# Performance work log

Measured on AMD Instinct MI355X. Metric: run time of the kernel, lower is better.

Reference implementation:

```python
import jax, jax.numpy as jnp
import numpy as np
import math

B, L, C, D, H, NL, DF, Z = 32, 256, 55, 512, 8, 3, 512, 16
DK = D // H


def setup_inputs() -> dict:
    key = jax.random.key(0)
    ks = iter(jax.random.split(key, 40))
    def w(shape, s=0.05):
        return jax.random.normal(next(ks), shape, jnp.float32) * s
    return {
        "x": jax.random.normal(next(ks), (B, L, C), jnp.float32),
        "tok_w": w((D, C, 3)),
        "qkv_w": w((NL, 3, D, D)), "qkv_b": w((NL, 3, D)),
        "sig_w": w((NL, H, D)), "sig_b": w((NL, H)),
        "out_w": w((NL, D, D)), "out_b": w((NL, D)),
        "conv1_w": w((NL, DF, D)), "conv1_b": w((NL, DF)),
        "conv2_w": w((NL, D, DF)), "conv2_b": w((NL, D)),
        "ln1_g": jnp.ones((NL, D)), "ln1_b": jnp.zeros((NL, D)),
        "ln2_g": jnp.ones((NL, D)), "ln2_b": jnp.zeros((NL, D)),
        "lnf_g": jnp.ones((D,)), "lnf_b": jnp.zeros((D,)),
        "lat_w": w((Z, D)), "lat_b": w((Z,)),
        "dec1_w": w((D, Z)), "dec1_b": w((D,)),
        "dec2_w": w((C, D)), "dec2_b": w((C,)),
    }


def _layer_norm(x, g, b, eps=1e-5):
    m = jnp.mean(x, axis=-1, keepdims=True)
    v = jnp.mean(jnp.square(x - m), axis=-1, keepdims=True)
    return (x - m) * jax.lax.rsqrt(v + eps) * g + b


def _pos_embedding(seq_len, d_model):
    pos = jnp.arange(seq_len, dtype=jnp.float32)[:, None]
    div = jnp.exp(jnp.arange(0, d_model, 2, dtype=jnp.float32) * (-math.log(10000.0) / d_model))
    pe = jnp.zeros((seq_len, d_model), jnp.float32)
    pe = pe.at[:, 0::2].set(jnp.sin(pos * div))
    pe = pe.at[:, 1::2].set(jnp.cos(pos * div))
    return pe  # (L, D)


def _token_embedding(x, tok_w):
    # torch Conv1d(C, D, k=3, padding=1, padding_mode='circular', bias=False)
    xp = jnp.pad(x, ((0, 0), (1, 1), (0, 0)), mode="wrap")  # circular pad on L
    k = jnp.transpose(tok_w, (2, 1, 0))  # (W=3, I=C, O=D)
    return jax.lax.conv_general_dilated(xp, k, (1,), "VALID",
                                        dimension_numbers=("NWC", "WIO", "NWC"))


def _forward(x, tok_w, qkv_w, qkv_b, sig_w, sig_b, out_w, out_b,
             conv1_w, conv1_b, conv2_w, conv2_b, ln1_g, ln1_b, ln2_g, ln2_b,
             lnf_g, lnf_b, lat_w, lat_b, dec1_w, dec1_b, dec2_w, dec2_b):
    Bx, Lx, _ = x.shape
    # DataEmbedding (dropout=0)
    h = _token_embedding(x, tok_w) + _pos_embedding(Lx, D)[None]
    dist = jnp.abs(jnp.arange(Lx, dtype=jnp.float32)[:, None]
                   - jnp.arange(Lx, dtype=jnp.float32)[None, :])  # (L, L)
    scale = 1.0 / math.sqrt(DK)
    series_list, prior_list = [], []
    for i in range(NL):
        # AttentionLayer projections
        q = (h @ qkv_w[i, 0].T + qkv_b[i, 0]).reshape(Bx, Lx, H, DK)
        k = (h @ qkv_w[i, 1].T + qkv_b[i, 1]).reshape(Bx, Lx, H, DK)
        v = (h @ qkv_w[i, 2].T + qkv_b[i, 2]).reshape(Bx, Lx, H, DK)
        sigma = h @ sig_w[i].T + sig_b[i]                 # (B, L, H)
        # AnomalyAttention
        scores = jnp.einsum("blhe,bshe->bhls", q, k) * scale
        series = jax.nn.softmax(scores, axis=-1)          # (B, H, L, L)
        sig = jnp.transpose(sigma, (0, 2, 1))             # (B, H, L)
        sig = jax.nn.sigmoid(sig * 5.0) + 1e-5
        sig = jnp.power(3.0, sig) - 1.0
        sig = sig[..., None]                              # (B, H, L, 1)
        prior = (1.0 / (math.sqrt(2.0 * math.pi) * sig)
                 * jnp.exp(-jnp.square(dist) / (2.0 * jnp.square(sig))))
        V = jnp.einsum("bhls,bshd->blhd", series, v).reshape(Bx, Lx, D)
        new_h = V @ out_w[i].T + out_b[i]
        # EncoderLayer (post-norm, pointwise-conv FFN, gelu)
        h = h + new_h
        y = h = _layer_norm(h, ln1_g[i], ln1_b[i])
        y = jax.nn.gelu(jnp.einsum("bld,fd->blf", y, conv1_w[i]) + conv1_b[i], approximate=False)
        y = jnp.einsum("blf,df->bld", y, conv2_w[i]) + conv2_b[i]
        h = _layer_norm(h + y, ln2_g[i], ln2_b[i])
        series_list.append(series)
        prior_list.append(prior)
    h = _layer_norm(h, lnf_g, lnf_b)
    z = h @ lat_w.T + lat_b                               # (B, L, Z)
    recon = jax.nn.relu(z @ dec1_w.T + dec1_b) @ dec2_w.T + dec2_b  # MLPDecoder
    return recon, jnp.stack(series_list), jnp.stack(prior_list), z


def reference(x, tok_w, qkv_w, qkv_b, sig_w, sig_b, out_w, out_b,
              conv1_w, conv1_b, conv2_w, conv2_b, ln1_g, ln1_b, ln2_g, ln2_b,
              lnf_g, lnf_b, lat_w, lat_b, dec1_w, dec1_b, dec2_w, dec2_b):
    return _forward(x, tok_w, qkv_w, qkv_b, sig_w, sig_b, out_w, out_b,
                    conv1_w, conv1_b, conv2_w, conv2_b, ln1_g, ln1_b, ln2_g, ln2_b,
                    lnf_g, lnf_b, lat_w, lat_b, dec1_w, dec1_b, dec2_w, dec2_b)
```

## Files before the change

### kernel.cpp

```cpp
#include <hip/hip_runtime.h>
#include <math.h>

#define B_ 32
#define L_ 256
#define C_ 55
#define D_ 512
#define H_ 8
#define NL_ 3
#define DF_ 512
#define Z_ 16
#define DK_ 64

typedef unsigned short u16;
typedef __attribute__((ext_vector_type(8))) short s16x8;
typedef __attribute__((ext_vector_type(8))) _Float16 f16x8;
typedef __attribute__((ext_vector_type(4))) float f32x4;

__device__ __forceinline__ u16 f2h(float f) {
  _Float16 h = (_Float16)f;
  return __builtin_bit_cast(u16, h);
}
__device__ __forceinline__ void gload16(const void* g, void* l) {
  __builtin_amdgcn_global_load_lds(
      (const __attribute__((address_space(1))) unsigned*)g,
      (__attribute__((address_space(3))) unsigned*)l, 16, 0, 0);
}

template <int MF, int WM, int WN, int ACT, int OUT>
__device__ __forceinline__ void mgemm_body(
    char* As, char* Bs, const u16* __restrict__ A16,
    const u16* __restrict__ B16, const float* __restrict__ bias,
    float* __restrict__ Cf, u16* __restrict__ C16, int K, int lda, int ldb,
    int ldc, int nmax, int bxi, int byi) {
  constexpr int BM = WM * MF * 16, BN = WN * 64, T = WM * WN * 64;
  constexpr int ACH = BM * 8, BCH = BN * 8;
  const int t = threadIdx.x, lane = t & 63, w = t >> 6;
  const int wm = w / WN, wn = w % WN;
  const long m0 = (long)byi * BM, n0 = (long)bxi * BN;
  const char* Ab = (const char*)(A16 + m0 * lda);
  const char* Bb = (const char*)(B16 + n0 * ldb);
  const int fr = lane & 15, gq = lane >> 4;
  const long lda2 = (long)lda * 2, ldb2 = (long)ldb * 2;
  f32x4 acc[MF][4] = {};
  for (int k0 = 0; k0 < K; k0 += 64) {
    const long kb = (long)k0 * 2;
#pragma unroll
    for (int e = 0; e < ACH; e += T) {
      int id = e + t;
      int row = id >> 3, c = (id & 7) ^ (row & 7);
      gload16(Ab + (long)row * lda2 + kb + c * 16, As + id * 16);
    }
#pragma unroll
    for (int e = 0; e < BCH; e += T) {
      int id = e + t;
      int row = id >> 3, c = (id & 7) ^ (row & 7);
      gload16(Bb + (long)row * ldb2 + kb + c * 16, Bs + id * 16);
    }
    __syncthreads();
#pragma unroll
    for (int ks = 0; ks < 2; ++ks) {
      f16x8 a[MF], b[4];
#pragma unroll
      for (int m = 0; m < MF; ++m) {
        int row = wm * (MF * 16) + m * 16 + fr;
        a[m] = *(const f16x8*)(As + row * 128 +
                               ((gq * 16 + ks * 64) ^ ((row & 7) << 4)));
      }
#pragma unroll
      for (int n = 0; n < 4; ++n) {
        int row = wn * 64 + n * 16 + fr;
        b[n] = *(const f16x8*)(Bs + row * 128 +
                               ((gq * 16 + ks * 64) ^ ((row & 7) << 4)));
      }
#pragma unroll
      for (int m = 0; m < MF; ++m)
#pragma unroll
        for (int n = 0; n < 4; ++n)
          acc[m][n] =
              __builtin_amdgcn_mfma_f32_16x16x32_f16(a[m], b[n], acc[m][n], 0, 0, 0);
    }
    __syncthreads();
  }
#pragma unroll
  for (int m = 0; m < MF; ++m) {
    long mg = m0 + wm * (MF * 16) + m * 16 + gq * 4;
#pragma unroll
    for (int n = 0; n < 4; ++n) {
      int ng = (int)n0 + wn * 64 + n * 16 + fr;
      if (ng >= nmax) continue;
      float bv = bias ? bias[ng] : 0.f;
#pragma unroll
      for (int r = 0; r < 4; ++r) {
        float v = acc[m][n][r] + bv;
        if (ACT == 1) v = 0.5f * v * (1.f + erff(v * 0.70710678118654752f));
        long idx = (mg + r) * ldc + ng;
        if (OUT == 0) Cf[idx] = v;
        if (OUT == 1) C16[idx] = f2h(v);
      }
    }
  }
}

template <int MF, int WM, int WN, int ACT, int OUT>
__global__ __launch_bounds__(WM * WN * 64) void mgemm(
    const u16* __restrict__ A16, const u16* __restrict__ B16,
    const float* __restrict__ bias, float* __restrict__ Cf,
    u16* __restrict__ C16, int K, int lda, int ldb, int ldc, int nmax) {
  __shared__ __align__(16) char As[WM * MF * 16 * 128];
  __shared__ __align__(16) char Bs[WN * 64 * 128];
  mgemm_body<MF, WM, WN, ACT, OUT>(As, Bs, A16, B16, bias, Cf, C16, K, lda,
                                   ldb, ldc, nmax, blockIdx.x, blockIdx.y);
}

__global__ __launch_bounds__(256) void qkv_kernel(
    const u16* __restrict__ h16, const u16* __restrict__ w16,
    const float* __restrict__ bias, u16* __restrict__ qk16,
    u16* __restrict__ vt16, const float* __restrict__ h32,
    const float* __restrict__ sw, const float* __restrict__ sb,
    float* __restrict__ coef, float* __restrict__ c2f) {
  __shared__ __align__(16) char As[128 * 128];
  __shared__ __align__(16) char Bs[128 * 128];
  __shared__ float sm[4][8];
  int bx = blockIdx.x;
  if (bx < 8192) {
    int bl = bx;
    int l = bl & 255, b = bl >> 8;
    int t = threadIdx.x;
    const float* hrow = h32 + (long)bl * 512;
    float h0 = hrow[t], h1 = hrow[t + 256];
    float part[8];
#pragma unroll
    for (int hd = 0; hd < 8; ++hd) {
      const float* wrow = sw + hd * 512;
      part[hd] = h0 * wrow[t] + h1 * wrow[t + 256];
    }
#pragma unroll
    for (int off = 32; off > 0; off >>= 1)
#pragma unroll
      for (int hd = 0; hd < 8; ++hd) part[hd] += __shfl_xor(part[hd], off, 64);
    int wid = t >> 6;
    if ((t & 63) == 0) {
#pragma unroll
      for (int hd = 0; hd < 8; ++hd) sm[wid][hd] = part[hd];
    }
    __syncthreads();
    if (t < 8) {
      float sig = sm[0][t] + sm[1][t] + sm[2][t] + sm[3][t] + sb[t];
      sig = 1.f / (1.f + expf(-5.f * sig));
      sig += 1e-5f;
      sig = expf(sig * 1.0986122886681098f) - 1.f;
      long idx = ((long)(b * 8 + t) << 8) | l;
      coef[idx] = 0.3989422804014327f / sig;
      c2f[idx] = -0.5f / (sig * sig);
    }
  } else if (bx < 8704) {
    int b2 = bx - 8192;
    mgemm_body<4, 2, 2, 0, 1>(As, Bs, h16, w16, bias, nullptr, qk16, 512, 512,
                              512, 1024, 1024, b2 & 7, b2 >> 3);
  } else {
    int b3 = bx - 8704;
    mgemm_body<2, 2, 2, 0, 1>(As, Bs, w16 + 1024 * 512, h16, nullptr, nullptr,
                              vt16, 512, 512, 512, 8192, 8192, b3 & 63,
                              b3 >> 6);
  }
}

__global__ __launch_bounds__(256, 2) void fused_attn(
    const u16* __restrict__ qk16, const u16* __restrict__ vt16,
    const float* __restrict__ vbias, const float* __restrict__ coef,
    const float* __restrict__ c2f, float* __restrict__ ser,
    float* __restrict__ pri, u16* __restrict__ pv16) {
  __shared__ __align__(16) char smem[67584];
  char* Kreg = smem;
  char* V0 = smem + 32768;
  char* V1 = smem + 49152;
  float* rowred = (float*)(smem + 65536);
  const int t = threadIdx.x, lane = t & 63, w = t >> 6;
  const int fr = lane & 15, gq = lane >> 4;
  const int r0 = blockIdx.x * 64;
  const int bh = blockIdx.y, b = bh >> 3, h = bh & 7;
  const long qrow0 = (long)b * 256 + r0;
  const long krow0 = (long)b * 256;
  {
    const char* qs = (const char*)qk16 + qrow0 * 2048 + h * 128;
#pragma unroll
    for (int j = 0; j < 2; ++j) {
      int id = t + j * 256;
      int row = id >> 3, c = id & 7;
      *(s16x8*)(V0 + row * 144 + c * 16) =
          *(const s16x8*)(qs + (long)row * 2048 + c * 16);
    }
  }
  const char* kb = (const char*)qk16 + krow0 * 2048 + 1024 + h * 128;
#pragma unroll
  for (int j = 0; j < 8; ++j) {
    int id = t + j * 256;
    int row = id >> 3, c = (id & 7) ^ (row & 7);
    gload16(kb + (long)row * 2048 + c * 16, Kreg + id * 16);
  }
  __syncthreads();
  f32x4 acc[4][4] = {};
#pragma unroll
  for (int ks = 0; ks < 2; ++ks) {
    f16x8 aq[4], bk[4];
#pragma unroll
    for (int m = 0; m < 4; ++m)
      aq[m] = *(const f16x8*)(V0 + (m * 16 + fr) * 144 + gq * 16 + ks * 64);
#pragma unroll
    for (int n = 0; n < 4; ++n) {
      int row = w * 64 + n * 16 + fr;
      bk[n] = *(const f16x8*)(Kreg + row * 128 +
                              ((gq * 16 + ks * 64) ^ ((row & 7) << 4)));
    }
#pragma unroll
    for (int m = 0; m < 4; ++m)
#pragma unroll
      for (int n = 0; n < 4; ++n)
        acc[m][n] =
            __builtin_amdgcn_mfma_f32_16x16x32_f16(aq[m], bk[n], acc[m][n], 0, 0, 0);
  }
#pragma unroll
  for (int m = 0; m < 4; ++m)
#pragma unroll
    for (int n = 0; n < 4; ++n) acc[m][n] *= 0.125f;
  float lmax[4][4], lsum[4][4];
#pragma unroll
  for (int m = 0; m < 4; ++m)
#pragma unroll
    for (int r = 0; r < 4; ++r) {
      float v = fmaxf(fmaxf(acc[m][0][r], acc[m][1][r]),
                      fmaxf(acc[m][2][r], acc[m][3][r]));
#pragma unroll
      for (int off = 8; off > 0; off >>= 1) v = fmaxf(v, __shfl_xor(v, off, 64));
      lmax[m][r] = v;
    }
#pragma unroll
  for (int m = 0; m < 4; ++m)
#pragma unroll
    for (int n = 0; n < 4; ++n)
#pragma unroll
      for (int r = 0; r < 4; ++r)
        acc[m][n][r] = __expf(acc[m][n][r] - lmax[m][r]);
#pragma unroll
  for (int m = 0; m < 4; ++m)
#pragma unroll
    for (int r = 0; r < 4; ++r) {
      float s = acc[m][0][r] + acc[m][1][r] + acc[m][2][r] + acc[m][3][r];
#pragma unroll
      for (int off = 8; off > 0; off >>= 1) s += __shfl_xor(s, off, 64);
      lsum[m][r] = s;
    }
  if (fr == 0) {
#pragma unroll
    for (int m = 0; m < 4; ++m)
#pragma unroll
      for (int r = 0; r < 4; ++r) {
        int row = m * 16 + gq * 4 + r;
        rowred[(w * 64 + row) * 2] = lmax[m][r];
        rowred[(w * 64 + row) * 2 + 1] = lsum[m][r];
      }
  }
  __syncthreads();
  float scale[4][4];
#pragma unroll
  for (int m = 0; m < 4; ++m)
#pragma unroll
    for (int r = 0; r < 4; ++r) {
      int row = m * 16 + gq * 4 + r;
      float g = -1e30f, tot = 0.f;
      float2 pr[4];
#pragma unroll
      for (int ww = 0; ww < 4; ++ww) {
        pr[ww] = *(const float2*)&rowred[(ww * 64 + row) * 2];
        g = fmaxf(g, pr[ww].x);
      }
#pragma unroll
      for (int ww = 0; ww < 4; ++ww) tot += pr[ww].y * __expf(pr[ww].x - g);
      scale[m][r] = __expf(lmax[m][r] - g) / tot;
    }
  const char* vtb = (const char*)vt16 + ((long)h * 64 * 8192 + krow0) * 2;
#pragma unroll
  for (int j = 0; j < 4; ++j) {
    int id = t + j * 256;
    int row = id >> 5, c = (id & 31) ^ (row & 7);
    gload16(vtb + (long)row * 16384 + c * 16, V0 + id * 16);
    gload16(vtb + (long)(32 + row) * 16384 + c * 16, V1 + id * 16);
  }
  float* serb = ser + ((long)bh * 256 + r0) * 256 + w * 64;
  float* prib = pri + ((long)bh * 256 + r0) * 256 + w * 64;
  const float* cfb = coef + bh * 256 + r0;
  const float* ccb = c2f + bh * 256 + r0;
#pragma unroll
  for (int m = 0; m < 4; ++m)
#pragma unroll
    for (int r = 0; r < 4; ++r) {
      int row = m * 16 + gq * 4 + r;
      float cf = cfb[row], cc = ccb[row];
      float fl = (float)(r0 + row);
#pragma unroll
      for (int n = 0; n < 4; ++n) {
        int col = n * 16 + fr;
        float p = acc[m][n][r] * scale[m][r];
        serb[(long)row * 256 + col] = p;
        int pb = row * 512 + (((w * 64 + col) * 2) ^ ((row & 7) << 4));
        *(u16*)(Kreg + pb) = f2h(p);
        float dd = fl - (float)(w * 64 + col);
        prib[(long)row * 256 + col] = cf * __expf(cc * dd * dd);
      }
    }
  __syncthreads();
  f32x4 acc2[2][2] = {};
#pragma unroll
  for (int ks = 0; ks < 8; ++ks) {
    int arow = w * 16 + fr;
    f16x8 pa = *(const f16x8*)(
        Kreg + arow * 512 + ((gq * 16 + ks * 64) ^ ((arow & 7) << 4)));
#pragma unroll
    for (int n = 0; n < 2; ++n) {
      int vrow = n * 16 + fr;
      int vo = vrow * 512 + ((gq * 16 + ks * 64) ^ ((vrow & 7) << 4));
      f16x8 vb0 = *(const f16x8*)(V0 + vo);
      f16x8 vb1 = *(const f16x8*)(V1 + vo);
      acc2[0][n] = __builtin_amdgcn_mfma_f32_16x16x32_f16(pa, vb0, acc2[0][n], 0, 0, 0);
      acc2[1][n] = __builtin_amdgcn_mfma_f32_16x16x32_f16(pa, vb1, acc2[1][n], 0, 0, 0);
    }
  }
#pragma unroll
  for (int half = 0; half < 2; ++half)
#pragma unroll
    for (int n = 0; n < 2; ++n)
#pragma unroll
      for (int r = 0; r < 4; ++r) {
        int gcol = h * 64 + half * 32 + n * 16 + fr;
        long gm = qrow0 + w * 16 + gq * 4 + r;
        pv16[gm * 512 + gcol] = f2h(acc2[half][n][r] + vbias[gcol]);
      }
}

template <int ACT, bool O16>
__global__ __launch_bounds__(256) void gemm_kernel(
    const float* __restrict__ A, const float* __restrict__ Bm,
    const float* __restrict__ bias, float* __restrict__ C,
    u16* __restrict__ C16, int M, int N, int K, int lda, int ldb, int ldc) {
  __shared__ float Asm[16][65];
  __shared__ float Bsm[16][65];
  int t = threadIdx.x;
  int tx = t & 15, ty = t >> 4;
  int n0 = blockIdx.x * 64, m0 = blockIdx.y * 64;
  float acc[4][4] = {};
  for (int k0 = 0; k0 < K; k0 += 16) {
#pragma unroll
    for (int e = 0; e < 4; ++e) {
      int idx = t + e * 256;
      int mi = idx >> 4, ki = idx & 15;
      int m = m0 + mi, kk = k0 + ki;
      Asm[ki][mi] = (m < M && kk < K) ? A[(long)m * lda + kk] : 0.f;
      int n = n0 + mi;
      Bsm[ki][mi] = (n < N && kk < K) ? Bm[(long)n * ldb + kk] : 0.f;
    }
    __syncthreads();
#pragma unroll
    for (int kk = 0; kk < 16; ++kk) {
      float a[4], b[4];
#pragma unroll
      for (int i = 0; i < 4; ++i) a[i] = Asm[kk][ty + 16 * i];
#pragma unroll
      for (int j = 0; j < 4; ++j) b[j] = Bsm[kk][tx + 16 * j];
#pragma unroll
      for (int i = 0; i < 4; ++i)
#pragma unroll
        for (int j = 0; j < 4; ++j) acc[i][j] = fmaf(a[i], b[j], acc[i][j]);
    }
    __syncthreads();
  }
#pragma unroll
  for (int i = 0; i < 4; ++i) {
    int m = m0 + ty + 16 * i;
    if (m >= M) continue;
#pragma unroll
    for (int j = 0; j < 4; ++j) {
      int n = n0 + tx + 16 * j;
      if (n >= N) continue;
      float v = acc[i][j];
      if (bias) v += bias[n];
      if (ACT == 2) v = fmaxf(v, 0.f);
      if (O16)
        C16[(long)m * ldc + n] = f2h(v);
      else
        C[(long)m * ldc + n] = v;
    }
  }
}

__global__ __launch_bounds__(256) void conv_embed_kernel(
    const float* __restrict__ x, const float* __restrict__ tw,
    const float* __restrict__ qkv_w, const float* __restrict__ out_w,
    const float* __restrict__ c1w, const float* __restrict__ c2w,
    const float* __restrict__ latw, const float* __restrict__ d2w,
    float* __restrict__ h32, u16* __restrict__ h16, u16* __restrict__ wqkv16,
    u16* __restrict__ wo16, u16* __restrict__ c116, u16* __restrict__ c216,
    u16* __restrict__ latpad, u16* __restrict__ d2pad) {
  __shared__ float xs[18][56];
  int bx = blockIdx.x;
  int t = threadIdx.x;
  if (bx < 512) {
    int lt = (bx & 15) * 16;
    int b = bx >> 4;
    for (int idx = t; idx < 18 * 55; idx += 256) {
      int rr = idx / 55, cc = idx % 55;
      int gl = (lt + rr - 1 + L_) & (L_ - 1);
      xs[rr][cc] = x[(long)(b * L_ + gl) * C_ + cc];
    }
    __syncthreads();
    for (int dp = 0; dp < 2; ++dp) {
      int d = t + dp * 256;
      float acc[16] = {};
      const float* wr = tw + (long)d * (C_ * 3);
      for (int c = 0; c < C_; ++c) {
#pragma unroll
        for (int w = 0; w < 3; ++w) {
          float wv = wr[c * 3 + w];
#pragma unroll
          for (int l = 0; l < 16; ++l) acc[l] = fmaf(xs[l + w][c], wv, acc[l]);
        }
      }
      float ang_scale = expf(-(float)(d & ~1) * 0.017988946039015984f);
#pragma unroll
      for (int l = 0; l < 16; ++l) {
        float ang = (float)(lt + l) * ang_scale;
        float pe = (d & 1) ? cosf(ang) : sinf(ang);
        float v = acc[l] + pe;
        long idx = (long)(b * L_ + lt + l) * D_ + d;
        h32[idx] = v;
        h16[idx] = f2h(v);
      }
    }
    return;
  }
  int cb = bx - 512;
  if (cb < 9216) {
    int i = cb * 256 + t;
    wqkv16[i] = f2h(qkv_w[i]);
  } else if (cb < 12288) {
    int i = (cb - 9216) * 256 + t;
    wo16[i] = f2h(out_w[i]);
  } else if (cb < 15360) {
    int i = (cb - 12288) * 256 + t;
    c116[i] = f2h(c1w[i]);
  } else if (cb < 18432) {
    int i = (cb - 15360) * 256 + t;
    c216[i] = f2h(c2w[i]);
  } else if (cb < 18560) {
    int i = (cb - 18432) * 256 + t;
    int r = i >> 9, c = i & 511;
    latpad[i] = (r < Z_) ? f2h(latw[r * 512 + c]) : (u16)0;
  } else {
    int i = (cb - 18560) * 256 + t;
    int r = i >> 9, c = i & 511;
    d2pad[i] = (r < C_) ? f2h(d2w[r * 512 + c]) : (u16)0;
  }
}

__global__ __launch_bounds__(256) void lnw_kernel(
    const float* __restrict__ a, const float* __restrict__ r,
    const float* __restrict__ gg, const float* __restrict__ be,
    float* __restrict__ ofp, u16* __restrict__ o16,
    const float* __restrict__ g2, const float* __restrict__ b2) {
  int wave = threadIdx.x >> 6, lane = threadIdx.x & 63;
  long row = (long)blockIdx.x * 4 + wave;
  long base = row * D_ + lane * 8;
  int cb = lane * 8;
  f32x4 xa = *(const f32x4*)(a + base);
  f32x4 xb = *(const f32x4*)(a + base + 4);
  if (r) {
    xa += *(const f32x4*)(r + base);
    xb += *(const f32x4*)(r + base + 4);
  }
  float x[8] = {xa.x, xa.y, xa.z, xa.w, xb.x, xb.y, xb.z, xb.w};
  float s = 0.f;
#pragma unroll
  for (int e = 0; e < 8; ++e) s += x[e];
#pragma unroll
  for (int off = 32; off > 0; off >>= 1) s += __shfl_xor(s, off, 64);
  float mean = s * (1.f / D_);
  float vv = 0.f;
#pragma unroll
  for (int e = 0; e < 8; ++e) {
    x[e] -= mean;
    vv += x[e] * x[e];
  }
#pragma unroll
  for (int off = 32; off > 0; off >>= 1) vv += __shfl_xor(vv, off, 64);
  float rstd = rsqrtf(vv * (1.f / D_) + 1e-5f);
  f32x4 ga = *(const f32x4*)(gg + cb), gb = *(const f32x4*)(gg + cb + 4);
  f32x4 ba = *(const f32x4*)(be + cb), bb = *(const f32x4*)(be + cb + 4);
  float g[8] = {ga.x, ga.y, ga.z, ga.w, gb.x, gb.y, gb.z, gb.w};
  float bi[8] = {ba.x, ba.y, ba.z, ba.w, bb.x, bb.y, bb.z, bb.w};
  float v[8];
#pragma unroll
  for (int e = 0; e < 8; ++e) v[e] = x[e] * rstd * g[e] + bi[e];
  if (ofp) {
    f32x4 oa = {v[0], v[1], v[2], v[3]}, ob = {v[4], v[5], v[6], v[7]};
    *(f32x4*)(ofp + base) = oa;
    *(f32x4*)(ofp + base + 4) = ob;
  }
  if (g2) {
    float s2 = 0.f;
#pragma unroll
    for (int e = 0; e < 8; ++e) s2 += v[e];
#pragma unroll
    for (int off = 32; off > 0; off >>= 1) s2 += __shfl_xor(s2, off, 64);
    float mean2 = s2 * (1.f / D_);
    float vv2 = 0.f;
#pragma unroll
    for (int e = 0; e < 8; ++e) {
      v[e] -= mean2;
      vv2 += v[e] * v[e];
    }
#pragma unroll
    for (int off = 32; off > 0; off >>= 1) vv2 += __shfl_xor(vv2, off, 64);
    float rstd2 = rsqrtf(vv2 * (1.f / D_) + 1e-5f);
    f32x4 g2a = *(const f32x4*)(g2 + cb), g2b = *(const f32x4*)(g2 + cb + 4);
    f32x4 b2a = *(const f32x4*)(b2 + cb), b2b = *(const f32x4*)(b2 + cb + 4);
    float gg2[8] = {g2a.x, g2a.y, g2a.z, g2a.w, g2b.x, g2b.y, g2b.z, g2b.w};
    float bb2[8] = {b2a.x, b2a.y, b2a.z, b2a.w, b2b.x, b2b.y, b2b.z, b2b.w};
#pragma unroll
    for (int e = 0; e < 8; ++e) v[e] = v[e] * rstd2 * gg2[e] + bb2[e];
  }
  if (o16) {
    u16 h[8];
#pragma unroll
    for (int e = 0; e < 8; ++e) h[e] = f2h(v[e]);
    *(s16x8*)(o16 + base) = *(s16x8*)h;
  }
}

extern "C" void kernel_launch(void* const* d_in, const int* in_sizes, int n_in,
                              void* d_out, int out_size, void* d_ws,
                              size_t ws_size, hipStream_t stream) {
  (void)in_sizes; (void)n_in; (void)out_size; (void)ws_size;
  const float* x = (const float*)d_in[0];
  const float* tok_w = (const float*)d_in[1];
  const float* qkv_w = (const float*)d_in[2];
  const float* qkv_b = (const float*)d_in[3];
  const float* sig_w = (const float*)d_in[4];
  const float* sig_b = (const float*)d_in[5];
  const float* out_w = (const float*)d_in[6];
  const float* out_b = (const float*)d_in[7];
  const float* c1w = (const float*)d_in[8];
  const float* c1b = (const float*)d_in[9];
  const float* c2w = (const float*)d_in[10];
  const float* c2b = (const float*)d_in[11];
  const float* ln1g = (const float*)d_in[12];
  const float* ln1b = (const float*)d_in[13];
  const float* ln2g = (const float*)d_in[14];
  const float* ln2b = (const float*)d_in[15];
  const float* lnfg = (const float*)d_in[16];
  const float* lnfb = (const float*)d_in[17];
  const float* latw = (const float*)d_in[18];
  const float* latb = (const float*)d_in[19];
  const float* d1w = (const float*)d_in[20];
  const float* d1b = (const float*)d_in[21];
  const float* d2w = (const float*)d_in[22];
  const float* d2b = (const float*)d_in[23];
  float* out = (float*)d_out;

  const long BLD = (long)B_ * L_ * D_;
  const long CHUNK = (long)B_ * H_ * L_ * L_;
  const long SER_OFF = (long)B_ * L_ * C_;
  const long PRI_OFF = SER_OFF + NL_ * CHUNK;
  const long Z_OFF = PRI_OFF + NL_ * CHUNK;
  const int M = B_ * L_;
  const int DD = D_ * D_;

  char* wp = (char*)d_ws;
  auto alloc = [&](size_t bytes) {
    char* p = wp;
    wp += (bytes + 255) & ~(size_t)255;
    return p;
  };
  float* h32 = (float*)alloc(BLD * 4);
  u16* h16 = (u16*)alloc(BLD * 2);
  float* tb = (float*)alloc(BLD * 4);
  u16* qk16 = (u16*)alloc(BLD * 4);
  u16* vt16 = (u16*)alloc(BLD * 2);
  u16* pv16 = (u16*)alloc(BLD * 2);
  float* coef = (float*)alloc((size_t)B_ * H_ * L_ * 4);
  float* c2f = (float*)alloc((size_t)B_ * H_ * L_ * 4);
  u16* wqkv16 = (u16*)alloc((size_t)NL_ * 3 * DD * 2);
  u16* wo16 = (u16*)alloc((size_t)NL_ * DD * 2);
  u16* c116 = (u16*)alloc((size_t)NL_ * DD * 2);
  u16* c216 = (u16*)alloc((size_t)NL_ * DD * 2);
  u16* latpad = (u16*)alloc((size_t)64 * 512 * 2);
  u16* d2pad = (u16*)alloc((size_t)64 * 512 * 2);

  conv_embed_kernel<<<18688, 256, 0, stream>>>(
      x, tok_w, qkv_w, out_w, c1w, c2w, latw, d2w, h32, h16, wqkv16, wo16,
      c116, c216, latpad, d2pad);

  for (int i = 0; i < NL_; ++i) {
    const long ofQK = (long)(i * 3) * DD;
    qkv_kernel<<<9216, 256, 0, stream>>>(
        h16, wqkv16 + ofQK, qkv_b + (long)i * 3 * D_, qk16, vt16, h32,
        sig_w + (long)i * H_ * D_, sig_b + i * H_, coef, c2f);
    fused_attn<<<dim3(4, 256), 256, 0, stream>>>(
        qk16, vt16, qkv_b + (long)(i * 3 + 2) * D_, coef, c2f,
        out + SER_OFF + i * CHUNK, out + PRI_OFF + i * CHUNK, pv16);
    mgemm<2, 2, 1, 0, 0><<<dim3(8, 128), 128, 0, stream>>>(
        pv16, wo16 + (long)i * DD, out_b + i * D_, tb, nullptr, D_, D_, D_, D_,
        D_);
    lnw_kernel<<<M / 4, 256, 0, stream>>>(h32, tb, ln1g + i * D_,
                                          ln1b + i * D_, h32, h16, nullptr,
                                          nullptr);
    u16* y16 = qk16;
    mgemm<2, 2, 1, 1, 1><<<dim3(8, 128), 128, 0, stream>>>(
        h16, c116 + (long)i * DD, c1b + i * DF_, nullptr, y16, D_, D_, D_, DF_,
        DF_);
    mgemm<2, 2, 1, 0, 0><<<dim3(8, 128), 128, 0, stream>>>(
        y16, c216 + (long)i * DD, c2b + i * D_, tb, nullptr, DF_, DF_, DF_, D_,
        D_);
    bool last = (i == NL_ - 1);
    lnw_kernel<<<M / 4, 256, 0, stream>>>(
        h32, tb, ln2g + i * D_, ln2b + i * D_, last ? nullptr : h32, h16,
        last ? lnfg : nullptr, last ? lnfb : nullptr);
  }
  mgemm<2, 2, 1, 0, 0><<<dim3(1, 128), 128, 0, stream>>>(
      h16, latpad, latb, out + Z_OFF, nullptr, D_, D_, D_, Z_, Z_);
  u16* dec16 = vt16;
  gemm_kernel<2, true><<<dim3(8, 128), 256, 0, stream>>>(
      out + Z_OFF, d1w, d1b, nullptr, dec16, M, D_, Z_, Z_, Z_, D_);
  mgemm<2, 2, 1, 0, 0><<<dim3(1, 128), 128, 0, stream>>>(
      dec16, d2pad, d2b, out, nullptr, D_, D_, D_, C_, C_);
}
```

Baseline: 640.5 us.

## Fuse output-projection and FFN2 GEMMs with residual add and LayerNorm

Adds a gemm_ln kernel where each 512-thread block computes 32 full rows of the 512-wide GEMM output, then adds bias and residual and applies LayerNorm (optionally a second final LN) in-register. This replaces the mgemm+lnw_kernel pairs and removes the fp32 temporary buffer round trip and two launches per layer. In exchange, each block streams the whole weight matrix through LDS, and only 256 blocks run, which lowers parallelism.

```diff
diff --git a/kernel.cpp b/kernel.cpp
--- a/kernel.cpp
+++ b/kernel.cpp
@@ -110,6 +110,243 @@
   __shared__ __align__(16) char Bs[WN * 64 * 128];
   mgemm_body<MF, WM, WN, ACT, OUT>(As, Bs, A16, B16, bias, Cf, C16, K, lda,
                                    ldb, ldc, nmax, blockIdx.x, blockIdx.y);
+}
+
+__global__ __launch_bounds__(512) void gemm_ln(
+    const u16* __restrict__ A16, const u16* __restrict__ B16,
+    const float* __restrict__ bias, const float* __restrict__ rowres,
+    const float* __restrict__ g1, const float* __restrict__ b1,
+    const float* __restrict__ g2, const float* __restrict__ b2,
+    float* __restrict__ h32o, u16* __restrict__ h16o) {
+  __shared__ __align__(16) char As[32 * 128];
+  __shared__ __align__(16) char Bs[512 * 128];
+  __shared__ float red[8][32];
+  const int t = threadIdx.x, lane = t & 63, w = t >> 6;
+  const int fr = lane & 15, gq = lane >> 4;
+  const long m0 = (long)blockIdx.x * 32;
+  const char* Ab = (const char*)(A16 + m0 * 512);
+  const char* Bb = (const char*)B16;
+  f32x4 acc[2][4] = {};
+  for (int k0 = 0; k0 < 512; k0 += 64) {
+    const long kb = (long)k0 * 2;
+    if (t < 256) {
+      int row = t >> 3, c = (t & 7) ^ (row & 7);
+      gload16(Ab + (long)row * 1024 + kb + c * 16, As + t * 16);
+    }
+#pragma unroll
+    for (int e = 0; e < 4096; e += 512) {
+      int id = e + t;
+      int row = id >> 3, c = (id & 7) ^ (row & 7);
+      gload16(Bb + (long)row * 1024 + kb + c * 16, Bs + id * 16);
+    }
+    __syncthreads();
+#pragma unroll
+    for (int ks = 0; ks < 2; ++ks) {
+      f16x8 a[2], b[4];
+#pragma unroll
+      for (int m = 0; m < 2; ++m) {
+        int row = m * 16 + fr;
+        a[m] = *(const f16x8*)(As + row * 128 +
+                               ((gq * 16 + ks * 64) ^ ((row & 7) << 4)));
+      }
+#pragma unroll
+      for (int n = 0; n < 4; ++n) {
+        int row = w * 64 + n * 16 + fr;
+        b[n] = *(const f16x8*)(Bs + row * 128 +
+                               ((gq * 16 + ks * 64) ^ ((row & 7) << 4)));
+      }
+#pragma unroll
+      for (int m = 0; m < 2; ++m)
+#pragma unroll
+        for (int n = 0; n < 4; ++n)
+          acc[m][n] =
+              __builtin_amdgcn_mfma_f32_16x16x32_f16(a[m], b[n], acc[m][n], 0, 0, 0);
+    }
+    __syncthreads();
+  }
+  float xv[2][4][4];
+#pragma unroll
+  for (int m = 0; m < 2; ++m)
+#pragma unroll
+    for (int n = 0; n < 4; ++n) {
+      int col = w * 64 + n * 16 + fr;
+      float bv = bias[col];
+#pragma unroll
+      for (int r = 0; r < 4; ++r) {
+        long row = m0 + m * 16 + gq * 4 + r;
+        xv[m][n][r] = acc[m][n][r] + bv + rowres[row * 512 + col];
+      }
+    }
+  float mean[2][4];
+  {
+    float ps[2][4];
+#pragma unroll
+    for (int m = 0; m < 2; ++m)
+#pragma unroll
+      for (int r = 0; r < 4; ++r) {
+        float s = xv[m][0][r] + xv[m][1][r] + xv[m][2][r] + xv[m][3][r];
+#pragma unroll
+        for (int off = 8; off > 0; off >>= 1) s += __shfl_xor(s, off, 64);
+        ps[m][r] = s;
+      }
+    if (fr == 0) {
+#pragma unroll
+      for (int m = 0; m < 2; ++m)
+#pragma unroll
+        for (int r = 0; r < 4; ++r) red[w][m * 16 + gq * 4 + r] = ps[m][r];
+    }
+    __syncthreads();
+#pragma unroll
+    for (int m = 0; m < 2; ++m)
+#pragma unroll
+      for (int r = 0; r < 4; ++r) {
+        int row = m * 16 + gq * 4 + r;
+        float s = red[0][row] + red[1][row] + red[2][row] + red[3][row] +
+                  red[4][row] + red[5][row] + red[6][row] + red[7][row];
+        mean[m][r] = s * (1.f / D_);
+      }
+    __syncthreads();
+  }
+  float rstd[2][4];
+  {
+    float ps[2][4];
+#pragma unroll
+    for (int m = 0; m < 2; ++m)
+#pragma unroll
+      for (int r = 0; r < 4; ++r) {
+        float s = 0.f;
+#pragma unroll
+        for (int n = 0; n < 4; ++n) {
+          float d = xv[m][n][r] - mean[m][r];
+          s += d * d;
+        }
+#pragma unroll
+        for (int off = 8; off > 0; off >>= 1) s += __shfl_xor(s, off, 64);
+        ps[m][r] = s;
+      }
+    if (fr == 0) {
+#pragma unroll
+      for (int m = 0; m < 2; ++m)
+#pragma unroll
+        for (int r = 0; r < 4; ++r) red[w][m * 16 + gq * 4 + r] = ps[m][r];
+    }
+    __syncthreads();
+#pragma unroll
+    for (int m = 0; m < 2; ++m)
+#pragma unroll
+      for (int r = 0; r < 4; ++r) {
+        int row = m * 16 + gq * 4 + r;
+        float s = red[0][row] + red[1][row] + red[2][row] + red[3][row] +
+                  red[4][row] + red[5][row] + red[6][row] + red[7][row];
+        rstd[m][r] = rsqrtf(s * (1.f / D_) + 1e-5f);
+      }
+    __syncthreads();
+  }
+  float vv[2][4][4];
+#pragma unroll
+  for (int m = 0; m < 2; ++m)
+#pragma unroll
+    for (int n = 0; n < 4; ++n) {
+      int col = w * 64 + n * 16 + fr;
+      float gv = g1[col], bv = b1[col];
+#pragma unroll
+      for (int r = 0; r < 4; ++r)
+        vv[m][n][r] = (xv[m][n][r] - mean[m][r]) * rstd[m][r] * gv + bv;
+    }
+  if (h32o) {
+#pragma unroll
+    for (int m = 0; m < 2; ++m)
+#pragma unroll
+      for (int n = 0; n < 4; ++n) {
+        int col = w * 64 + n * 16 + fr;
+#pragma unroll
+        for (int r = 0; r < 4; ++r) {
+          long row = m0 + m * 16 + gq * 4 + r;
+          h32o[row * 512 + col] = vv[m][n][r];
+        }
+      }
+  }
+  if (g2) {
+    float mean2[2][4], rstd2[2][4];
+    float ps[2][4];
+#pragma unroll
+    for (int m = 0; m < 2; ++m)
+#pragma unroll
+      for (int r = 0; r < 4; ++r) {
+        float s = vv[m][0][r] + vv[m][1][r] + vv[m][2][r] + vv[m][3][r];
+#pragma unroll
+        for (int off = 8; off > 0; off >>= 1) s += __shfl_xor(s, off, 64);
+        ps[m][r] = s;
+      }
+    if (fr == 0) {
+#pragma unroll
+      for (int m = 0; m < 2; ++m)
+#pragma unroll
+        for (int r = 0; r < 4; ++r) red[w][m * 16 + gq * 4 + r] = ps[m][r];
+    }
+    __syncthreads();
+#pragma unroll
+    for (int m = 0; m < 2; ++m)
+#pragma unroll
+      for (int r = 0; r < 4; ++r) {
+        int row = m * 16 + gq * 4 + r;
+        float s = red[0][row] + red[1][row] + red[2][row] + red[3][row] +
+                  red[4][row] + red[5][row] + red[6][row] + red[7][row];
+        mean2[m][r] = s * (1.f / D_);
+      }
+    __syncthreads();
+#pragma unroll
+    for (int m = 0; m < 2; ++m)
+#pragma unroll
+      for (int r = 0; r < 4; ++r) {
+        float s = 0.f;
+#pragma unroll
+        for (int n = 0; n < 4; ++n) {
+          float d = vv[m][n][r] - mean2[m][r];
+          s += d * d;
+        }
+#pragma unroll
+        for (int off = 8; off > 0; off >>= 1) s += __shfl_xor(s, off, 64);
+        ps[m][r] = s;
+      }
+    if (fr == 0) {
+#pragma unroll
+      for (int m = 0; m < 2; ++m)
+#pragma unroll
+        for (int r = 0; r < 4; ++r) red[w][m * 16 + gq * 4 + r] = ps[m][r];
+    }
+    __syncthreads();
+#pragma unroll
+    for (int m = 0; m < 2; ++m)
+#pragma unroll
+      for (int r = 0; r < 4; ++r) {
+        int row = m * 16 + gq * 4 + r;
+        float s = red[0][row] + red[1][row] + red[2][row] + red[3][row] +
+                  red[4][row] + red[5][row] + red[6][row] + red[7][row];
+        rstd2[m][r] = rsqrtf(s * (1.f / D_) + 1e-5f);
+      }
+#pragma unroll
+    for (int m = 0; m < 2; ++m)
+#pragma unroll
+      for (int n = 0; n < 4; ++n) {
+        int col = w * 64 + n * 16 + fr;
+        float gv = g2[col], bv = b2[col];
+#pragma unroll
+        for (int r = 0; r < 4; ++r)
+          vv[m][n][r] = (vv[m][n][r] - mean2[m][r]) * rstd2[m][r] * gv + bv;
+      }
+  }
+#pragma unroll
+  for (int m = 0; m < 2; ++m)
+#pragma unroll
+    for (int n = 0; n < 4; ++n) {
+      int col = w * 64 + n * 16 + fr;
+#pragma unroll
+      for (int r = 0; r < 4; ++r) {
+        long row = m0 + m * 16 + gq * 4 + r;
+        h16o[row * 512 + col] = f2h(vv[m][n][r]);
+      }
+    }
 }
 
 __global__ __launch_bounds__(256) void qkv_kernel(
@@ -458,80 +695,6 @@
     int i = (cb - 18560) * 256 + t;
     int r = i >> 9, c = i & 511;
     d2pad[i] = (r < C_) ? f2h(d2w[r * 512 + c]) : (u16)0;
-  }
-}
-
-__global__ __launch_bounds__(256) void lnw_kernel(
-    const float* __restrict__ a, const float* __restrict__ r,
-    const float* __restrict__ gg, const float* __restrict__ be,
-    float* __restrict__ ofp, u16* __restrict__ o16,
-    const float* __restrict__ g2, const float* __restrict__ b2) {
-  int wave = threadIdx.x >> 6, lane = threadIdx.x & 63;
-  long row = (long)blockIdx.x * 4 + wave;
-  long base = row * D_ + lane * 8;
-  int cb = lane * 8;
-  f32x4 xa = *(const f32x4*)(a + base);
-  f32x4 xb = *(const f32x4*)(a + base + 4);
-  if (r) {
-    xa += *(const f32x4*)(r + base);
-    xb += *(const f32x4*)(r + base + 4);
-  }
-  float x[8] = {xa.x, xa.y, xa.z, xa.w, xb.x, xb.y, xb.z, xb.w};
-  float s = 0.f;
-#pragma unroll
-  for (int e = 0; e < 8; ++e) s += x[e];
-#pragma unroll
-  for (int off = 32; off > 0; off >>= 1) s += __shfl_xor(s, off, 64);
-  float mean = s * (1.f / D_);
-  float vv = 0.f;
-#pragma unroll
-  for (int e = 0; e < 8; ++e) {
-    x[e] -= mean;
-    vv += x[e] * x[e];
-  }
-#pragma unroll
-  for (int off = 32; off > 0; off >>= 1) vv += __shfl_xor(vv, off, 64);
-  float rstd = rsqrtf(vv * (1.f / D_) + 1e-5f);
-  f32x4 ga = *(const f32x4*)(gg + cb), gb = *(const f32x4*)(gg + cb + 4);
-  f32x4 ba = *(const f32x4*)(be + cb), bb = *(const f32x4*)(be + cb + 4);
-  float g[8] = {ga.x, ga.y, ga.z, ga.w, gb.x, gb.y, gb.z, gb.w};
-  float bi[8] = {ba.x, ba.y, ba.z, ba.w, bb.x, bb.y, bb.z, bb.w};
-  float v[8];
-#pragma unroll
-  for (int e = 0; e < 8; ++e) v[e] = x[e] * rstd * g[e] + bi[e];
-  if (ofp) {
-    f32x4 oa = {v[0], v[1], v[2], v[3]}, ob = {v[4], v[5], v[6], v[7]};
-    *(f32x4*)(ofp + base) = oa;
-    *(f32x4*)(ofp + base + 4) = ob;
-  }
-  if (g2) {
-    float s2 = 0.f;
-#pragma unroll
-    for (int e = 0; e < 8; ++e) s2 += v[e];
-#pragma unroll
-    for (int off = 32; off > 0; off >>= 1) s2 += __shfl_xor(s2, off, 64);
-    float mean2 = s2 * (1.f / D_);
-    float vv2 = 0.f;
-#pragma unroll
-    for (int e = 0; e < 8; ++e) {
-      v[e] -= mean2;
-      vv2 += v[e] * v[e];
-    }
-#pragma unroll
-    for (int off = 32; off > 0; off >>= 1) vv2 += __shfl_xor(vv2, off, 64);
-    float rstd2 = rsqrtf(vv2 * (1.f / D_) + 1e-5f);
-    f32x4 g2a = *(const f32x4*)(g2 + cb), g2b = *(const f32x4*)(g2 + cb + 4);
-    f32x4 b2a = *(const f32x4*)(b2 + cb), b2b = *(const f32x4*)(b2 + cb + 4);
-    float gg2[8] = {g2a.x, g2a.y, g2a.z, g2a.w, g2b.x, g2b.y, g2b.z, g2b.w};
-    float bb2[8] = {b2a.x, b2a.y, b2a.z, b2a.w, b2b.x, b2b.y, b2b.z, b2b.w};
-#pragma unroll
-    for (int e = 0; e < 8; ++e) v[e] = v[e] * rstd2 * gg2[e] + bb2[e];
-  }
-  if (o16) {
-    u16 h[8];
-#pragma unroll
-    for (int e = 0; e < 8; ++e) h[e] = f2h(v[e]);
-    *(s16x8*)(o16 + base) = *(s16x8*)h;
   }
 }
 
@@ -581,7 +744,6 @@
   };
   float* h32 = (float*)alloc(BLD * 4);
   u16* h16 = (u16*)alloc(BLD * 2);
-  float* tb = (float*)alloc(BLD * 4);
   u16* qk16 = (u16*)alloc(BLD * 4);
   u16* vt16 = (u16*)alloc(BLD * 2);
   u16* pv16 = (u16*)alloc(BLD * 2);
@@ -606,23 +768,18 @@
     fused_attn<<<dim3(4, 256), 256, 0, stream>>>(
         qk16, vt16, qkv_b + (long)(i * 3 + 2) * D_, coef, c2f,
         out + SER_OFF + i * CHUNK, out + PRI_OFF + i * CHUNK, pv16);
-    mgemm<2, 2, 1, 0, 0><<<dim3(8, 128), 128, 0, stream>>>(
-        pv16, wo16 + (long)i * DD, out_b + i * D_, tb, nullptr, D_, D_, D_, D_,
-        D_);
-    lnw_kernel<<<M / 4, 256, 0, stream>>>(h32, tb, ln1g + i * D_,
-                                          ln1b + i * D_, h32, h16, nullptr,
-                                          nullptr);
+    gemm_ln<<<256, 512, 0, stream>>>(pv16, wo16 + (long)i * DD, out_b + i * D_,
+                                     h32, ln1g + i * D_, ln1b + i * D_,
+                                     nullptr, nullptr, h32, h16);
     u16* y16 = qk16;
     mgemm<2, 2, 1, 1, 1><<<dim3(8, 128), 128, 0, stream>>>(
         h16, c116 + (long)i * DD, c1b + i * DF_, nullptr, y16, D_, D_, D_, DF_,
         DF_);
-    mgemm<2, 2, 1, 0, 0><<<dim3(8, 128), 128, 0, stream>>>(
-        y16, c216 + (long)i * DD, c2b + i * D_, tb, nullptr, DF_, DF_, DF_, D_,
-        D_);
     bool last = (i == NL_ - 1);
-    lnw_kernel<<<M / 4, 256, 0, stream>>>(
-        h32, tb, ln2g + i * D_, ln2b + i * D_, last ? nullptr : h32, h16,
-        last ? lnfg : nullptr, last ? lnfb : nullptr);
+    gemm_ln<<<256, 512, 0, stream>>>(
+        y16, c216 + (long)i * DD, c2b + i * D_, h32, ln2g + i * D_,
+        ln2b + i * D_, last ? lnfg : nullptr, last ? lnfb : nullptr,
+        last ? nullptr : h32, h16);
   }
   mgemm<2, 2, 1, 0, 0><<<dim3(1, 128), 128, 0, stream>>>(
       h16, latpad, latb, out + Z_OFF, nullptr, D_, D_, D_, Z_, Z_);
```

Result: slower. 661.1 us (+3.2%).
